# Kernel tuning notes

Hardware: AMD Instinct MI355X
Metric: run time of the kernel (lower is better)

Reference implementation:

```python
import jax, jax.numpy as jnp
import numpy as np

B, H = 32, 1024  # seq_len == hidden_size (required by the original code's shapes)
S = H

def setup_inputs() -> dict:
    key = jax.random.key(0)
    k1, k2, k3, k4, k5 = jax.random.split(key, 5)
    hidden = jax.random.normal(k1, (B, H), dtype=jnp.float32)
    encoder_outputs = jax.random.normal(k2, (B, S, H), dtype=jnp.float32)
    # nn.Linear(2H -> H): weight [H, 2H], bias [H]
    lim = 1.0 / np.sqrt(2 * H)
    W = jax.random.uniform(k3, (H, 2 * H), dtype=jnp.float32, minval=-lim, maxval=lim)
    b = jax.random.uniform(k4, (H,), dtype=jnp.float32, minval=-lim, maxval=lim)
    # v ~ Normal(0, 1/H)
    v = jax.random.normal(k5, (H,), dtype=jnp.float32) * (1.0 / H)
    return {"hidden": hidden, "encoder_outputs": encoder_outputs, "W": W, "b": b, "v": v}

def reference(hidden, encoder_outputs, W, b, v):
    # hidden: [B, H]; encoder_outputs: [B, S, H] with S == H
    S_len = encoder_outputs.shape[1]
    h_rep = jnp.broadcast_to(hidden[:, None, :], (hidden.shape[0], S_len, hidden.shape[1]))
    enc_t = jnp.swapaxes(encoder_outputs, 1, 2)  # [B, H, S] == [B, S, H] (square)
    x = jnp.concatenate([h_rep, enc_t], axis=2)  # [B, S, 2H]
    energy = jnp.tanh(jnp.einsum('bsk,hk->bsh', x, W) + b)  # [B, S, H]
    # scores[b,s] = sum_h v[h] * energy[b,s,h], softmax over s
    scores = jax.nn.softmax(jnp.einsum('h,bsh->bs', v, energy), axis=1)  # [B, S]
    # bmm(scores[B,1,S], enc_t.transpose(1,2)=encoder_outputs[B,S,H]) -> [B, H]
    context = jnp.einsum('bs,bsh->bh', scores, encoder_outputs)
    return context, scores[:, None, :]
```

## Files before the change

### kernel.cpp

```cpp
#include <hip/hip_runtime.h>
#include <hip/hip_bf16.h>
#include <math.h>

#define B_ 32
#define H_ 1024
#define S_ 1024

typedef __bf16 bf16x4_t __attribute__((ext_vector_type(4)));
typedef __bf16 bf16x8_t __attribute__((ext_vector_type(8)));
typedef float  f32x4_t  __attribute__((ext_vector_type(4)));
typedef float  f32x16_t __attribute__((ext_vector_type(16)));

__device__ __forceinline__ void gl_lds16(const void* g, void* l) {
    __builtin_amdgcn_global_load_lds(
        (const __attribute__((address_space(1))) uint32_t*)g,
        (__attribute__((address_space(3))) uint32_t*)l,
        16, 0, 0);
}

__device__ __forceinline__ float tanh_fast(float x) {
    float e = __builtin_amdgcn_exp2f(x * 2.885390081777927f);
    return 1.f - 2.f * __builtin_amdgcn_rcpf(e + 1.f);
}

__global__ __launch_bounds__(256) void term1_kernel(
    const float* __restrict__ hidden, const float* __restrict__ W,
    const float* __restrict__ bias, float* __restrict__ t1)
{
    int h    = blockIdx.x * 4 + (threadIdx.x >> 6);
    int lane = threadIdx.x & 63;
    const float4* wp = reinterpret_cast<const float4*>(W + (size_t)h * (2 * H_));
    float4 w0 = wp[lane], w1 = wp[lane + 64], w2 = wp[lane + 128], w3 = wp[lane + 192];
    float bh = bias[h];
    for (int b = 0; b < B_; ++b) {
        const float4* hp = reinterpret_cast<const float4*>(hidden + b * H_);
        float4 h0 = hp[lane], h1 = hp[lane + 64], h2 = hp[lane + 128], h3 = hp[lane + 192];
        float a = w0.x*h0.x + w0.y*h0.y + w0.z*h0.z + w0.w*h0.w
                + w1.x*h1.x + w1.y*h1.y + w1.z*h1.z + w1.w*h1.w
                + w2.x*h2.x + w2.y*h2.y + w2.z*h2.z + w2.w*h2.w
                + w3.x*h3.x + w3.y*h3.y + w3.z*h3.z + w3.w*h3.w;
        #pragma unroll
        for (int off = 1; off < 64; off <<= 1) a += __shfl_xor(a, off);
        if (lane == 0) t1[b * H_ + h] = a + bh;
    }
}

__global__ __launch_bounds__(256) void prep_kernel(
    const float* __restrict__ enc, const float* __restrict__ W,
    __bf16* __restrict__ encT, __bf16* __restrict__ W2b)
{
    __shared__ float T[64 * 65];
    const int idx = blockIdx.x;
    const int tid = threadIdx.x;
    if (idx < 8192) {
        const int b  = idx >> 8;
        const int k0 = ((idx >> 4) & 15) * 64;
        const int s0 = (idx & 15) * 64;
        #pragma unroll
        for (int it = 0; it < 4; ++it) {
            int flat = tid + it * 256;
            int r = flat >> 4, c4 = flat & 15;
            float4 vv = *reinterpret_cast<const float4*>(
                enc + ((size_t)b * S_ + k0 + r) * H_ + s0 + c4 * 4);
            T[r * 65 + c4 * 4 + 0] = vv.x;
            T[r * 65 + c4 * 4 + 1] = vv.y;
            T[r * 65 + c4 * 4 + 2] = vv.z;
            T[r * 65 + c4 * 4 + 3] = vv.w;
        }
        __syncthreads();
        #pragma unroll
        for (int it = 0; it < 4; ++it) {
            int flat = tid + it * 256;
            int s = flat >> 4, kq = flat & 15;
            bf16x4_t p = { (__bf16)T[(kq * 4 + 0) * 65 + s],
                           (__bf16)T[(kq * 4 + 1) * 65 + s],
                           (__bf16)T[(kq * 4 + 2) * 65 + s],
                           (__bf16)T[(kq * 4 + 3) * 65 + s] };
            *reinterpret_cast<bf16x4_t*>(
                encT + ((size_t)b * S_ + s0 + s) * H_ + k0 + kq * 4) = p;
        }
    } else {
        int i2 = (idx - 8192) * 1024 + tid * 4;
        int h = i2 >> 10, c = i2 & 1023;
        float4 vv = *reinterpret_cast<const float4*>(W + (size_t)h * (2 * H_) + H_ + c);
        bf16x4_t p = { (__bf16)vv.x, (__bf16)vv.y, (__bf16)vv.z, (__bf16)vv.w };
        *reinterpret_cast<bf16x4_t*>(W2b + (size_t)h * H_ + c) = p;
    }
}

#define BKE 64

__global__ __launch_bounds__(256) void energy_kernel(
    const __bf16* __restrict__ W2b, const __bf16* __restrict__ encT,
    const float* __restrict__ t1, const float* __restrict__ v,
    float* __restrict__ logits)
{
    __shared__ __align__(16) __bf16 As[128 * BKE];
    __shared__ __align__(16) __bf16 Bs[128 * BKE];

    const int b     = blockIdx.z;
    const int h0    = blockIdx.x * 128;
    const int s0    = blockIdx.y * 128;
    const int tid   = threadIdx.x;
    const int lane  = tid & 63;
    const int wid   = tid >> 6;
    const int wm    = (wid & 1) * 64;
    const int wn    = (wid >> 1) * 64;
    const int l32   = lane & 31;
    const int khalf = lane >> 5;

    const __bf16* gAp[4]; const __bf16* gBp[4];
    __bf16* lAp[4]; __bf16* lBp[4];
    #pragma unroll
    for (int i = 0; i < 4; ++i) {
        int f   = tid + i * 256;
        int row = f >> 3;
        int c   = (f & 7) ^ (row & 7);
        gAp[i] = W2b + (size_t)(h0 + row) * H_ + c * 8;
        gBp[i] = encT + ((size_t)b * S_ + s0 + row) * H_ + c * 8;
        lAp[i] = As + f * 8;
        lBp[i] = Bs + f * 8;
    }

    f32x16_t acc[2][2] = {};

    for (int k0 = 0; k0 < H_; k0 += BKE) {
        #pragma unroll
        for (int i = 0; i < 4; ++i) gl_lds16(gAp[i] + k0, lAp[i]);
        #pragma unroll
        for (int i = 0; i < 4; ++i) gl_lds16(gBp[i] + k0, lBp[i]);
        __syncthreads();

        #pragma unroll
        for (int ks = 0; ks < 4; ++ks) {
            int p8 = (((khalf + 2 * ks) ^ (l32 & 7)) * 8);
            bf16x8_t a0 = *reinterpret_cast<const bf16x8_t*>(&As[(wm + l32) * BKE + p8]);
            bf16x8_t a1 = *reinterpret_cast<const bf16x8_t*>(&As[(wm + 32 + l32) * BKE + p8]);
            bf16x8_t b0 = *reinterpret_cast<const bf16x8_t*>(&Bs[(wn + l32) * BKE + p8]);
            bf16x8_t b1 = *reinterpret_cast<const bf16x8_t*>(&Bs[(wn + 32 + l32) * BKE + p8]);
            acc[0][0] = __builtin_amdgcn_mfma_f32_32x32x16_bf16(a0, b0, acc[0][0], 0, 0, 0);
            acc[0][1] = __builtin_amdgcn_mfma_f32_32x32x16_bf16(a0, b1, acc[0][1], 0, 0, 0);
            acc[1][0] = __builtin_amdgcn_mfma_f32_32x32x16_bf16(a1, b0, acc[1][0], 0, 0, 0);
            acc[1][1] = __builtin_amdgcn_mfma_f32_32x32x16_bf16(a1, b1, acc[1][1], 0, 0, 0);
        }
        __syncthreads();
    }

    float pn0 = 0.f, pn1 = 0.f;
    #pragma unroll
    for (int mt = 0; mt < 2; ++mt)
        #pragma unroll
        for (int r = 0; r < 16; ++r) {
            int row = wm + mt * 32 + (r & 3) + 8 * (r >> 2) + 4 * khalf;
            int h = h0 + row;
            float tv = t1[b * H_ + h];
            float vv = v[h];
            pn0 += vv * tanh_fast(acc[mt][0][r] + tv);
            pn1 += vv * tanh_fast(acc[mt][1][r] + tv);
        }
    pn0 += __shfl_xor(pn0, 32);
    pn1 += __shfl_xor(pn1, 32);
    if (lane < 32) {
        atomicAdd(&logits[(size_t)b * S_ + s0 + wn + l32], pn0);
        atomicAdd(&logits[(size_t)b * S_ + s0 + wn + 32 + l32], pn1);
    }
}

__global__ __launch_bounds__(256) void softmax_kernel(
    const float* __restrict__ logits, float* __restrict__ scores)
{
    int b = blockIdx.x, tid = threadIdx.x;
    float x[4];
    float mx = -3.4e38f;
    #pragma unroll
    for (int i = 0; i < 4; ++i) {
        x[i] = logits[b * S_ + tid + i * 256];
        mx = fmaxf(mx, x[i]);
    }
    #pragma unroll
    for (int off = 1; off < 64; off <<= 1) mx = fmaxf(mx, __shfl_xor(mx, off));
    __shared__ float sm[4], ss[4];
    if ((tid & 63) == 0) sm[tid >> 6] = mx;
    __syncthreads();
    mx = fmaxf(fmaxf(sm[0], sm[1]), fmaxf(sm[2], sm[3]));
    float s = 0.f;
    #pragma unroll
    for (int i = 0; i < 4; ++i) {
        x[i] = expf(x[i] - mx);
        s += x[i];
    }
    #pragma unroll
    for (int off = 1; off < 64; off <<= 1) s += __shfl_xor(s, off);
    if ((tid & 63) == 0) ss[tid >> 6] = s;
    __syncthreads();
    float inv = 1.f / (ss[0] + ss[1] + ss[2] + ss[3]);
    #pragma unroll
    for (int i = 0; i < 4; ++i)
        scores[b * S_ + tid + i * 256] = x[i] * inv;
}

__global__ __launch_bounds__(256) void context_kernel(
    const __bf16* __restrict__ encT, const float* __restrict__ scores,
    float* __restrict__ ctx)
{
    int gw   = blockIdx.x * 4 + (threadIdx.x >> 6);
    int b    = gw >> 10;
    int h    = gw & 1023;
    int lane = threadIdx.x & 63;
    const __bf16* rp = encT + ((size_t)b * S_ + h) * H_;
    const float*  sp = scores + (size_t)b * S_;
    float acc = 0.f;
    #pragma unroll
    for (int c = 0; c < 2; ++c) {
        int s8 = (lane + c * 64) * 8;
        bf16x8_t ev = *reinterpret_cast<const bf16x8_t*>(&rp[s8]);
        float4 sa = *reinterpret_cast<const float4*>(&sp[s8]);
        float4 sb = *reinterpret_cast<const float4*>(&sp[s8 + 4]);
        acc += (float)ev[0]*sa.x + (float)ev[1]*sa.y + (float)ev[2]*sa.z + (float)ev[3]*sa.w
             + (float)ev[4]*sb.x + (float)ev[5]*sb.y + (float)ev[6]*sb.z + (float)ev[7]*sb.w;
    }
    #pragma unroll
    for (int off = 1; off < 64; off <<= 1) acc += __shfl_xor(acc, off);
    if (lane == 0) ctx[(size_t)b * H_ + h] = acc;
}

extern "C" void kernel_launch(void* const* d_in, const int* in_sizes, int n_in,
                              void* d_out, int out_size, void* d_ws, size_t ws_size,
                              hipStream_t stream)
{
    (void)in_sizes; (void)n_in; (void)out_size; (void)ws_size;
    const float* hidden = (const float*)d_in[0];
    const float* enc    = (const float*)d_in[1];
    const float* W      = (const float*)d_in[2];
    const float* bias   = (const float*)d_in[3];
    const float* v      = (const float*)d_in[4];

    float* out    = (float*)d_out;
    float* ctx    = out;
    float* scores = out + B_ * H_;

    float*  logits = (float*)d_ws;
    float*  t1     = logits + B_ * S_;
    __bf16* W2b    = (__bf16*)(t1 + B_ * H_);
    __bf16* encT   = W2b + (size_t)H_ * H_;

    hipMemsetAsync(logits, 0, (size_t)B_ * S_ * sizeof(float), stream);

    term1_kernel<<<dim3(H_ / 4), 256, 0, stream>>>(hidden, W, bias, t1);
    prep_kernel<<<dim3(8192 + 1024), 256, 0, stream>>>(enc, W, encT, W2b);
    energy_kernel<<<dim3(H_ / 128, S_ / 128, B_), 256, 0, stream>>>(
        W2b, encT, t1, v, logits);
    softmax_kernel<<<B_, 256, 0, stream>>>(logits, scores);
    context_kernel<<<dim3(B_ * H_ / 4), 256, 0, stream>>>(encT, scores, ctx);
}
```

Before: 336.7 us.

## Double-buffer energy GEMM, fuse softmax into context, merge term1 into prep

The energy GEMM moves to double-buffered LDS tiles with K=32 per stage and a new swizzle, so global-to-LDS loads of the next tile overlap the current tile's MFMAs. The term1 kernel is folded into prep_kernel as extra blocks. The softmax kernel is folded into a new ctx_kernel that recomputes the softmax per block, stages the scores in LDS, and processes 16 rows per wave. The encoder transpose now writes 8-wide bf16 stores. The aim is fewer launches and less exposed load latency, at the cost of redundant softmax work per block and a thinner K stage per barrier.

New measurement: 328.3 us. 2.5% less time.

```diff
diff --git a/kernel.cpp b/kernel.cpp
--- a/kernel.cpp
+++ b/kernel.cpp
@@ -23,31 +23,11 @@
     return 1.f - 2.f * __builtin_amdgcn_rcpf(e + 1.f);
 }
 
-__global__ __launch_bounds__(256) void term1_kernel(
-    const float* __restrict__ hidden, const float* __restrict__ W,
-    const float* __restrict__ bias, float* __restrict__ t1)
-{
-    int h    = blockIdx.x * 4 + (threadIdx.x >> 6);
-    int lane = threadIdx.x & 63;
-    const float4* wp = reinterpret_cast<const float4*>(W + (size_t)h * (2 * H_));
-    float4 w0 = wp[lane], w1 = wp[lane + 64], w2 = wp[lane + 128], w3 = wp[lane + 192];
-    float bh = bias[h];
-    for (int b = 0; b < B_; ++b) {
-        const float4* hp = reinterpret_cast<const float4*>(hidden + b * H_);
-        float4 h0 = hp[lane], h1 = hp[lane + 64], h2 = hp[lane + 128], h3 = hp[lane + 192];
-        float a = w0.x*h0.x + w0.y*h0.y + w0.z*h0.z + w0.w*h0.w
-                + w1.x*h1.x + w1.y*h1.y + w1.z*h1.z + w1.w*h1.w
-                + w2.x*h2.x + w2.y*h2.y + w2.z*h2.z + w2.w*h2.w
-                + w3.x*h3.x + w3.y*h3.y + w3.z*h3.z + w3.w*h3.w;
-        #pragma unroll
-        for (int off = 1; off < 64; off <<= 1) a += __shfl_xor(a, off);
-        if (lane == 0) t1[b * H_ + h] = a + bh;
-    }
-}
-
 __global__ __launch_bounds__(256) void prep_kernel(
     const float* __restrict__ enc, const float* __restrict__ W,
-    __bf16* __restrict__ encT, __bf16* __restrict__ W2b)
+    const float* __restrict__ hidden, const float* __restrict__ bias,
+    __bf16* __restrict__ encT, __bf16* __restrict__ W2b,
+    float* __restrict__ t1)
 {
     __shared__ float T[64 * 65];
     const int idx = blockIdx.x;
@@ -69,34 +49,51 @@
         }
         __syncthreads();
         #pragma unroll
-        for (int it = 0; it < 4; ++it) {
+        for (int it = 0; it < 2; ++it) {
             int flat = tid + it * 256;
-            int s = flat >> 4, kq = flat & 15;
-            bf16x4_t p = { (__bf16)T[(kq * 4 + 0) * 65 + s],
-                           (__bf16)T[(kq * 4 + 1) * 65 + s],
-                           (__bf16)T[(kq * 4 + 2) * 65 + s],
-                           (__bf16)T[(kq * 4 + 3) * 65 + s] };
-            *reinterpret_cast<bf16x4_t*>(
-                encT + ((size_t)b * S_ + s0 + s) * H_ + k0 + kq * 4) = p;
-        }
-    } else {
+            int s = flat >> 3, ko = flat & 7;
+            bf16x8_t p;
+            #pragma unroll
+            for (int j = 0; j < 8; ++j)
+                p[j] = (__bf16)T[(ko * 8 + j) * 65 + s];
+            *reinterpret_cast<bf16x8_t*>(
+                encT + ((size_t)b * S_ + s0 + s) * H_ + k0 + ko * 8) = p;
+        }
+    } else if (idx < 9216) {
         int i2 = (idx - 8192) * 1024 + tid * 4;
         int h = i2 >> 10, c = i2 & 1023;
         float4 vv = *reinterpret_cast<const float4*>(W + (size_t)h * (2 * H_) + H_ + c);
         bf16x4_t p = { (__bf16)vv.x, (__bf16)vv.y, (__bf16)vv.z, (__bf16)vv.w };
         *reinterpret_cast<bf16x4_t*>(W2b + (size_t)h * H_ + c) = p;
-    }
-}
-
-#define BKE 64
+    } else {
+        int h    = (idx - 9216) * 4 + (tid >> 6);
+        int lane = tid & 63;
+        const float4* wp = reinterpret_cast<const float4*>(W + (size_t)h * (2 * H_));
+        float4 w0 = wp[lane], w1 = wp[lane + 64], w2 = wp[lane + 128], w3 = wp[lane + 192];
+        float bh = bias[h];
+        for (int b = 0; b < B_; ++b) {
+            const float4* hp = reinterpret_cast<const float4*>(hidden + b * H_);
+            float4 h0 = hp[lane], h1 = hp[lane + 64], h2 = hp[lane + 128], h3 = hp[lane + 192];
+            float a = w0.x*h0.x + w0.y*h0.y + w0.z*h0.z + w0.w*h0.w
+                    + w1.x*h1.x + w1.y*h1.y + w1.z*h1.z + w1.w*h1.w
+                    + w2.x*h2.x + w2.y*h2.y + w2.z*h2.z + w2.w*h2.w
+                    + w3.x*h3.x + w3.y*h3.y + w3.z*h3.z + w3.w*h3.w;
+            #pragma unroll
+            for (int off = 1; off < 64; off <<= 1) a += __shfl_xor(a, off);
+            if (lane == 0) t1[b * H_ + h] = a + bh;
+        }
+    }
+}
+
+#define BK2 32
 
 __global__ __launch_bounds__(256) void energy_kernel(
     const __bf16* __restrict__ W2b, const __bf16* __restrict__ encT,
     const float* __restrict__ t1, const float* __restrict__ v,
     float* __restrict__ logits)
 {
-    __shared__ __align__(16) __bf16 As[128 * BKE];
-    __shared__ __align__(16) __bf16 Bs[128 * BKE];
+    __shared__ __align__(16) __bf16 As[2][128 * BK2];
+    __shared__ __align__(16) __bf16 Bs[2][128 * BK2];
 
     const int b     = blockIdx.z;
     const int h0    = blockIdx.x * 128;
@@ -109,35 +106,44 @@
     const int l32   = lane & 31;
     const int khalf = lane >> 5;
 
-    const __bf16* gAp[4]; const __bf16* gBp[4];
-    __bf16* lAp[4]; __bf16* lBp[4];
-    #pragma unroll
-    for (int i = 0; i < 4; ++i) {
+    const __bf16* gA[2]; const __bf16* gB[2]; int lofs[2];
+    #pragma unroll
+    for (int i = 0; i < 2; ++i) {
         int f   = tid + i * 256;
-        int row = f >> 3;
-        int c   = (f & 7) ^ (row & 7);
-        gAp[i] = W2b + (size_t)(h0 + row) * H_ + c * 8;
-        gBp[i] = encT + ((size_t)b * S_ + s0 + row) * H_ + c * 8;
-        lAp[i] = As + f * 8;
-        lBp[i] = Bs + f * 8;
-    }
+        int row = f >> 2;
+        int c   = (f & 3) ^ ((row >> 3) & 3);
+        gA[i]   = W2b + (size_t)(h0 + row) * H_ + c * 8;
+        gB[i]   = encT + ((size_t)b * S_ + s0 + row) * H_ + c * 8;
+        lofs[i] = f * 8;
+    }
+
+    #pragma unroll
+    for (int i = 0; i < 2; ++i) {
+        gl_lds16(gA[i], &As[0][lofs[i]]);
+        gl_lds16(gB[i], &Bs[0][lofs[i]]);
+    }
+    __syncthreads();
 
     f32x16_t acc[2][2] = {};
-
-    for (int k0 = 0; k0 < H_; k0 += BKE) {
-        #pragma unroll
-        for (int i = 0; i < 4; ++i) gl_lds16(gAp[i] + k0, lAp[i]);
-        #pragma unroll
-        for (int i = 0; i < 4; ++i) gl_lds16(gBp[i] + k0, lBp[i]);
-        __syncthreads();
-
-        #pragma unroll
-        for (int ks = 0; ks < 4; ++ks) {
-            int p8 = (((khalf + 2 * ks) ^ (l32 & 7)) * 8);
-            bf16x8_t a0 = *reinterpret_cast<const bf16x8_t*>(&As[(wm + l32) * BKE + p8]);
-            bf16x8_t a1 = *reinterpret_cast<const bf16x8_t*>(&As[(wm + 32 + l32) * BKE + p8]);
-            bf16x8_t b0 = *reinterpret_cast<const bf16x8_t*>(&Bs[(wn + l32) * BKE + p8]);
-            bf16x8_t b1 = *reinterpret_cast<const bf16x8_t*>(&Bs[(wn + 32 + l32) * BKE + p8]);
+    const int pswz = (l32 >> 3) & 3;
+
+    for (int it = 0; it < H_ / BK2; ++it) {
+        const int cur = it & 1, nxt = cur ^ 1;
+        if (it < H_ / BK2 - 1) {
+            const int k1 = (it + 1) * BK2;
+            #pragma unroll
+            for (int i = 0; i < 2; ++i) {
+                gl_lds16(gA[i] + k1, &As[nxt][lofs[i]]);
+                gl_lds16(gB[i] + k1, &Bs[nxt][lofs[i]]);
+            }
+        }
+        #pragma unroll
+        for (int ks = 0; ks < 2; ++ks) {
+            int p8 = ((khalf + 2 * ks) ^ pswz) * 8;
+            bf16x8_t a0 = *reinterpret_cast<const bf16x8_t*>(&As[cur][(wm      + l32) * BK2 + p8]);
+            bf16x8_t a1 = *reinterpret_cast<const bf16x8_t*>(&As[cur][(wm + 32 + l32) * BK2 + p8]);
+            bf16x8_t b0 = *reinterpret_cast<const bf16x8_t*>(&Bs[cur][(wn      + l32) * BK2 + p8]);
+            bf16x8_t b1 = *reinterpret_cast<const bf16x8_t*>(&Bs[cur][(wn + 32 + l32) * BK2 + p8]);
             acc[0][0] = __builtin_amdgcn_mfma_f32_32x32x16_bf16(a0, b0, acc[0][0], 0, 0, 0);
             acc[0][1] = __builtin_amdgcn_mfma_f32_32x32x16_bf16(a0, b1, acc[0][1], 0, 0, 0);
             acc[1][0] = __builtin_amdgcn_mfma_f32_32x32x16_bf16(a1, b0, acc[1][0], 0, 0, 0);
@@ -166,62 +172,59 @@
     }
 }
 
-__global__ __launch_bounds__(256) void softmax_kernel(
-    const float* __restrict__ logits, float* __restrict__ scores)
-{
-    int b = blockIdx.x, tid = threadIdx.x;
-    float x[4];
-    float mx = -3.4e38f;
-    #pragma unroll
-    for (int i = 0; i < 4; ++i) {
-        x[i] = logits[b * S_ + tid + i * 256];
-        mx = fmaxf(mx, x[i]);
-    }
+__global__ __launch_bounds__(256) void ctx_kernel(
+    const __bf16* __restrict__ encT, const float* __restrict__ logits,
+    float* __restrict__ scores, float* __restrict__ ctx)
+{
+    __shared__ float sc[1024];
+    __shared__ float red[8];
+    const int b    = blockIdx.y;
+    const int hb   = blockIdx.x * 64;
+    const int tid  = threadIdx.x;
+    const int lane = tid & 63;
+    const int w    = tid >> 6;
+
+    float4 lg = *reinterpret_cast<const float4*>(logits + (size_t)b * S_ + tid * 4);
+    float mx = fmaxf(fmaxf(lg.x, lg.y), fmaxf(lg.z, lg.w));
     #pragma unroll
     for (int off = 1; off < 64; off <<= 1) mx = fmaxf(mx, __shfl_xor(mx, off));
-    __shared__ float sm[4], ss[4];
-    if ((tid & 63) == 0) sm[tid >> 6] = mx;
-    __syncthreads();
-    mx = fmaxf(fmaxf(sm[0], sm[1]), fmaxf(sm[2], sm[3]));
-    float s = 0.f;
-    #pragma unroll
-    for (int i = 0; i < 4; ++i) {
-        x[i] = expf(x[i] - mx);
-        s += x[i];
-    }
+    if (lane == 0) red[w] = mx;
+    __syncthreads();
+    mx = fmaxf(fmaxf(red[0], red[1]), fmaxf(red[2], red[3]));
+    const float L2E = 1.44269504088896f;
+    float e0 = __builtin_amdgcn_exp2f((lg.x - mx) * L2E);
+    float e1 = __builtin_amdgcn_exp2f((lg.y - mx) * L2E);
+    float e2 = __builtin_amdgcn_exp2f((lg.z - mx) * L2E);
+    float e3 = __builtin_amdgcn_exp2f((lg.w - mx) * L2E);
+    float s = e0 + e1 + e2 + e3;
     #pragma unroll
     for (int off = 1; off < 64; off <<= 1) s += __shfl_xor(s, off);
-    if ((tid & 63) == 0) ss[tid >> 6] = s;
-    __syncthreads();
-    float inv = 1.f / (ss[0] + ss[1] + ss[2] + ss[3]);
-    #pragma unroll
-    for (int i = 0; i < 4; ++i)
-        scores[b * S_ + tid + i * 256] = x[i] * inv;
-}
-
-__global__ __launch_bounds__(256) void context_kernel(
-    const __bf16* __restrict__ encT, const float* __restrict__ scores,
-    float* __restrict__ ctx)
-{
-    int gw   = blockIdx.x * 4 + (threadIdx.x >> 6);
-    int b    = gw >> 10;
-    int h    = gw & 1023;
-    int lane = threadIdx.x & 63;
-    const __bf16* rp = encT + ((size_t)b * S_ + h) * H_;
-    const float*  sp = scores + (size_t)b * S_;
-    float acc = 0.f;
-    #pragma unroll
-    for (int c = 0; c < 2; ++c) {
-        int s8 = (lane + c * 64) * 8;
-        bf16x8_t ev = *reinterpret_cast<const bf16x8_t*>(&rp[s8]);
-        float4 sa = *reinterpret_cast<const float4*>(&sp[s8]);
-        float4 sb = *reinterpret_cast<const float4*>(&sp[s8 + 4]);
-        acc += (float)ev[0]*sa.x + (float)ev[1]*sa.y + (float)ev[2]*sa.z + (float)ev[3]*sa.w
-             + (float)ev[4]*sb.x + (float)ev[5]*sb.y + (float)ev[6]*sb.z + (float)ev[7]*sb.w;
-    }
-    #pragma unroll
-    for (int off = 1; off < 64; off <<= 1) acc += __shfl_xor(acc, off);
-    if (lane == 0) ctx[(size_t)b * H_ + h] = acc;
+    if (lane == 0) red[4 + w] = s;
+    __syncthreads();
+    float inv = 1.f / (red[4] + red[5] + red[6] + red[7]);
+    float4 sv = { e0 * inv, e1 * inv, e2 * inv, e3 * inv };
+    *reinterpret_cast<float4*>(&sc[tid * 4]) = sv;
+    if (blockIdx.x == 0)
+        *reinterpret_cast<float4*>(scores + (size_t)b * S_ + tid * 4) = sv;
+    __syncthreads();
+
+    for (int r = 0; r < 16; ++r) {
+        int h = hb + w * 16 + r;
+        const __bf16* rp = encT + ((size_t)b * S_ + h) * H_;
+        float acc = 0.f;
+        #pragma unroll
+        for (int c = 0; c < 2; ++c) {
+            int s8 = (lane + c * 64) * 8;
+            bf16x8_t ev = *reinterpret_cast<const bf16x8_t*>(&rp[s8]);
+            float4 sa = *reinterpret_cast<const float4*>(&sc[s8]);
+            float4 sb = *reinterpret_cast<const float4*>(&sc[s8 + 4]);
+            acc += (float)ev[0]*sa.x + (float)ev[1]*sa.y + (float)ev[2]*sa.z + (float)ev[3]*sa.w
+                 + (float)ev[4]*sb.x + (float)ev[5]*sb.y + (float)ev[6]*sb.z + (float)ev[7]*sb.w;
+        }
+        #pragma unroll
+        for (int off = 1; off < 64; off <<= 1) acc += __shfl_xor(acc, off);
+        if (lane == 0) ctx[(size_t)b * H_ + h] = acc;
+    }
 }
 
 extern "C" void kernel_launch(void* const* d_in, const int* in_sizes, int n_in,
@@ -246,10 +249,9 @@
 
     hipMemsetAsync(logits, 0, (size_t)B_ * S_ * sizeof(float), stream);
 
-    term1_kernel<<<dim3(H_ / 4), 256, 0, stream>>>(hidden, W, bias, t1);
-    prep_kernel<<<dim3(8192 + 1024), 256, 0, stream>>>(enc, W, encT, W2b);
+    prep_kernel<<<dim3(8192 + 1024 + 256), 256, 0, stream>>>(
+        enc, W, hidden, bias, encT, W2b, t1);
     energy_kernel<<<dim3(H_ / 128, S_ / 128, B_), 256, 0, stream>>>(
         W2b, encT, t1, v, logits);
-    softmax_kernel<<<B_, 256, 0, stream>>>(logits, scores);
-    context_kernel<<<dim3(B_ * H_ / 4), 256, 0, stream>>>(encT, scores, ctx);
-}
+    ctx_kernel<<<dim3(H_ / 64, B_), 256, 0, stream>>>(encT, logits, scores, ctx);
+}
```
